# Kernel optimization log

Hardware: AMD Instinct MI355X
Metric: run time of the kernel (lower is better)

## Reference

```python
import jax, jax.numpy as jnp
import numpy as np

RX, RY = 10, 10  # box filter half-widths (Angle == 0 path)


def setup_inputs() -> dict:
    key = jax.random.key(0)
    x = jax.random.normal(key, (8, 1, 2048, 2048), dtype=jnp.float32)
    # Angle == 0: constant all-ones box kernel (1,1,2rx+1,2ry+1), a fixed buffer
    kernelx = jnp.ones((1, 1, 2 * RX + 1, 2 * RY + 1), dtype=jnp.float32)
    return {"x": x, "kernelx": kernelx}


def reference(x, kernelx):
    # circular pad: H by rx (top/bottom), W by ry (left/right), matching
    # F.pad(input, (ry, ry, rx, rx), mode='circular')
    xp = jnp.pad(x, ((0, 0), (0, 0), (RX, RX), (RY, RY)), mode="wrap")
    # valid conv with the box kernel -> output has the original HxW
    out = jax.lax.conv_general_dilated(
        xp, kernelx,
        window_strides=(1, 1),
        padding="VALID",
        dimension_numbers=("NCHW", "OIHW", "NCHW"),
    )
    return out
```

## Files before the change

### kernel.cpp

```cpp
#include <hip/hip_runtime.h>


#define HH 2048
#define WW 2048
#define RAD 10
#define DIAM 21
#define TH 64
#define TW 64
#define SIN_H (TH + 2 * RAD)
#define SIN_W (TW + 2 * RAD)
#define SIN_STRIDE (SIN_W + 1)
#define RS_STRIDE (TW + 1)

__global__ __launch_bounds__(256) void box_filter_kernel(
    const float* __restrict__ x, float* __restrict__ out) {
  __shared__ float sIn[SIN_H * SIN_STRIDE];
  __shared__ float sRS[SIN_H * RS_STRIDE];

  const int n = blockIdx.z;
  const int tile_h0 = blockIdx.y * TH;
  const int tile_w0 = blockIdx.x * TW;
  const float* __restrict__ xp = x + (size_t)n * HH * WW;
  float* __restrict__ op = out + (size_t)n * HH * WW;
  const int tid = threadIdx.x;

  for (int idx = tid; idx < SIN_H * SIN_W; idx += 256) {
    int i = idx / SIN_W;
    int j = idx - i * SIN_W;
    int gr = (tile_h0 + i - RAD) & (HH - 1);
    int gc = (tile_w0 + j - RAD) & (WW - 1);
    sIn[i * SIN_STRIDE + j] = xp[(size_t)gr * WW + gc];
  }
  __syncthreads();

  for (int t = tid; t < SIN_H * 4; t += 256) {
    int i = t >> 2;
    int jg = (t & 3) * 16;
    const float* row = &sIn[i * SIN_STRIDE];
    float* rsrow = &sRS[i * RS_STRIDE];
    float sum = 0.f;
#pragma unroll
    for (int k = 0; k < DIAM; ++k) sum += row[jg + k];
    rsrow[jg] = sum;
#pragma unroll
    for (int j = 1; j < 16; ++j) {
      sum += row[jg + j + DIAM - 1] - row[jg + j - 1];
      rsrow[jg + j] = sum;
    }
  }
  __syncthreads();

  {
    int j = tid & 63;
    int i0 = (tid >> 6) * 16;
    float sum = 0.f;
#pragma unroll
    for (int k = 0; k < DIAM; ++k) sum += sRS[(i0 + k) * RS_STRIDE + j];
    const int gc = tile_w0 + j;
    const int gr = tile_h0 + i0;
    op[(size_t)gr * WW + gc] = sum;
#pragma unroll
    for (int i = 1; i < 16; ++i) {
      sum += sRS[(i0 + i + DIAM - 1) * RS_STRIDE + j] -
             sRS[(i0 + i - 1) * RS_STRIDE + j];
      op[(size_t)(gr + i) * WW + gc] = sum;
    }
  }
}

extern "C" void kernel_launch(void* const* d_in, const int* in_sizes, int n_in,
                              void* d_out, int out_size, void* d_ws, size_t ws_size,
                              hipStream_t stream) {
  const float* x = (const float*)d_in[0];
  float* out = (float*)d_out;
  dim3 grid(WW / TW, HH / TH, 8);
  dim3 block(256);
  hipLaunchKernelGGL(box_filter_kernel, grid, block, 0, stream, x, out);
}
```

Baseline: 270.0 us.

## Do column pass straight from global memory and vectorize row-pass output stores

The separable box filter is reordered so the vertical sliding sum runs first. Each thread loads 36 consecutive rows of one column from global memory into registers and writes 16 column sums to shared memory, so the staging copy of the input tile disappears along with one shared buffer and one barrier. The horizontal pass reads 36 column sums per thread from shared memory into registers and writes 16 outputs with float4 stores instead of scalar strided stores. In exchange it uses more registers per thread (two 36-element arrays), and global loads stay scalar (one float per lane, coalesced across the wavefront).

Result: faster. 260.6 us (-3.5%).

```diff
diff --git a/kernel.cpp b/kernel.cpp
--- a/kernel.cpp
+++ b/kernel.cpp
@@ -7,64 +7,62 @@
 #define DIAM 21
 #define TH 64
 #define TW 64
-#define SIN_H (TH + 2 * RAD)
-#define SIN_W (TW + 2 * RAD)
-#define SIN_STRIDE (SIN_W + 1)
-#define RS_STRIDE (TW + 1)
+#define CS_W (TW + 2 * RAD)
+#define CS_STRIDE (CS_W + 1)
 
-__global__ __launch_bounds__(256) void box_filter_kernel(
+__global__ __launch_bounds__(256) void box_filter_v2(
     const float* __restrict__ x, float* __restrict__ out) {
-  __shared__ float sIn[SIN_H * SIN_STRIDE];
-  __shared__ float sRS[SIN_H * RS_STRIDE];
+  __shared__ float sCS[TH * CS_STRIDE];
 
   const int n = blockIdx.z;
-  const int tile_h0 = blockIdx.y * TH;
-  const int tile_w0 = blockIdx.x * TW;
+  const int h0 = blockIdx.y * TH;
+  const int w0 = blockIdx.x * TW;
   const float* __restrict__ xp = x + (size_t)n * HH * WW;
   float* __restrict__ op = out + (size_t)n * HH * WW;
   const int tid = threadIdx.x;
 
-  for (int idx = tid; idx < SIN_H * SIN_W; idx += 256) {
-    int i = idx / SIN_W;
-    int j = idx - i * SIN_W;
-    int gr = (tile_h0 + i - RAD) & (HH - 1);
-    int gc = (tile_w0 + j - RAD) & (WW - 1);
-    sIn[i * SIN_STRIDE + j] = xp[(size_t)gr * WW + gc];
-  }
-  __syncthreads();
-
-  for (int t = tid; t < SIN_H * 4; t += 256) {
-    int i = t >> 2;
-    int jg = (t & 3) * 16;
-    const float* row = &sIn[i * SIN_STRIDE];
-    float* rsrow = &sRS[i * RS_STRIDE];
-    float sum = 0.f;
+  for (int t = tid; t < CS_W * 4; t += 256) {
+    int c = t % CS_W;
+    int g = t / CS_W;
+    int gc = (w0 - RAD + c) & (WW - 1);
+    int rbase = h0 + 16 * g - RAD;
+    float v[36];
 #pragma unroll
-    for (int k = 0; k < DIAM; ++k) sum += row[jg + k];
-    rsrow[jg] = sum;
+    for (int k = 0; k < 36; ++k)
+      v[k] = xp[(size_t)((rbase + k) & (HH - 1)) * WW + gc];
+    float s = 0.f;
 #pragma unroll
-    for (int j = 1; j < 16; ++j) {
-      sum += row[jg + j + DIAM - 1] - row[jg + j - 1];
-      rsrow[jg + j] = sum;
+    for (int k = 0; k < DIAM; ++k) s += v[k];
+    sCS[(16 * g) * CS_STRIDE + c] = s;
+#pragma unroll
+    for (int i = 1; i < 16; ++i) {
+      s += v[i + DIAM - 1] - v[i - 1];
+      sCS[(16 * g + i) * CS_STRIDE + c] = s;
     }
   }
   __syncthreads();
 
   {
-    int j = tid & 63;
-    int i0 = (tid >> 6) * 16;
-    float sum = 0.f;
+    int r = tid >> 2;
+    int cg = tid & 3;
+    const float* csrow = &sCS[r * CS_STRIDE + cg * 16];
+    float w[36];
 #pragma unroll
-    for (int k = 0; k < DIAM; ++k) sum += sRS[(i0 + k) * RS_STRIDE + j];
-    const int gc = tile_w0 + j;
-    const int gr = tile_h0 + i0;
-    op[(size_t)gr * WW + gc] = sum;
+    for (int k = 0; k < 36; ++k) w[k] = csrow[k];
+    float o[16];
+    float s = 0.f;
 #pragma unroll
-    for (int i = 1; i < 16; ++i) {
-      sum += sRS[(i0 + i + DIAM - 1) * RS_STRIDE + j] -
-             sRS[(i0 + i - 1) * RS_STRIDE + j];
-      op[(size_t)(gr + i) * WW + gc] = sum;
+    for (int k = 0; k < DIAM; ++k) s += w[k];
+    o[0] = s;
+#pragma unroll
+    for (int j = 1; j < 16; ++j) {
+      s += w[j + DIAM - 1] - w[j - 1];
+      o[j] = s;
     }
+    float4* dst = (float4*)&op[(size_t)(h0 + r) * WW + w0 + cg * 16];
+#pragma unroll
+    for (int q = 0; q < 4; ++q)
+      dst[q] = make_float4(o[4 * q], o[4 * q + 1], o[4 * q + 2], o[4 * q + 3]);
   }
 }
 
@@ -75,5 +73,5 @@
   float* out = (float*)d_out;
   dim3 grid(WW / TW, HH / TH, 8);
   dim3 block(256);
-  hipLaunchKernelGGL(box_filter_kernel, grid, block, 0, stream, x, out);
+  hipLaunchKernelGGL(box_filter_v2, grid, block, 0, stream, x, out);
 }
```
